# Kernel tuning notes

Measured on AMD Instinct MI355X. Metric: run time of the kernel, lower is better.

Reference implementation:

```python
import jax, jax.numpy as jnp
import numpy as np

B, S, N_EMBD = 4, 4096, 1024
HIDDEN = 4 * N_EMBD
M_BITS_FC = 3
M_BITS_PROJ = 3
BLOCK_K = 32


def block_quant(v, m_bits, bk):
    """Block-floating-point quantization along the last (K) dim.
    Each block of `bk` elements shares an exponent derived from its max-abs;
    mantissas are rounded to `m_bits` bits. Straight-through estimator for grads."""
    *lead, K = v.shape
    vb = v.reshape(*lead, K // bk, bk)
    amax = jnp.max(jnp.abs(vb), axis=-1, keepdims=True)
    tiny = jnp.asarray(2.0 ** -126, v.dtype)
    e = jnp.floor(jnp.log2(jnp.maximum(amax, tiny)))  # shared block exponent
    scale = jnp.exp2(e - m_bits)                       # quantization step
    q = jnp.round(vb / scale) * scale
    q = vb + jax.lax.stop_gradient(q - vb)             # STE
    return q.reshape(v.shape)


def lowprec_linear(x, w, b, m_bits, bk):
    # w: [out, in]; quantize both operands along the contraction dim.
    xq = block_quant(x, m_bits, bk)
    wq = block_quant(w, m_bits, bk)
    return jnp.einsum('bsk,nk->bsn', xq, wq) + b


def setup_inputs() -> dict:
    key = jax.random.key(0)
    k0, k1, k2 = jax.random.split(key, 3)
    x = jax.random.normal(k0, (B, S, N_EMBD), jnp.float32)
    w_fc = jax.random.normal(k1, (HIDDEN, N_EMBD), jnp.float32) * (1.0 / np.sqrt(N_EMBD))
    b_fc = jnp.zeros((HIDDEN,), jnp.float32)
    w_proj = jax.random.normal(k2, (N_EMBD, HIDDEN), jnp.float32) * (1.0 / np.sqrt(HIDDEN))
    b_proj = jnp.zeros((N_EMBD,), jnp.float32)
    return {"x": x, "w_fc": w_fc, "b_fc": b_fc, "w_proj": w_proj, "b_proj": b_proj}


def reference(x, w_fc, b_fc, w_proj, b_proj):
    h = lowprec_linear(x, w_fc, b_fc, M_BITS_FC, BLOCK_K)
    h = jax.nn.gelu(h, approximate=False)  # nn.GELU default = exact erf
    return lowprec_linear(h, w_proj, b_proj, M_BITS_PROJ, BLOCK_K)
```

## Files before the change

### kernel.cpp

```cpp
#include <hip/hip_runtime.h>
#include <hip/hip_bf16.h>

using bf16 = __hip_bfloat16;
typedef __attribute__((ext_vector_type(8))) short short8;
typedef __attribute__((ext_vector_type(4))) float f32x4;

#define DI __device__ __forceinline__

constexpr int MROWS = 16384;
constexpr int EMB   = 1024;
constexpr int HID   = 4096;

DI void gload16(const bf16* g, bf16* l) {
  __builtin_amdgcn_global_load_lds((const __attribute__((address_space(1))) void*)g,
                                   (__attribute__((address_space(3))) void*)l,
                                   16, 0, 0);
}

DI void qparams(float amax, float& scale, float& inv) {
  int eb = (int)((__float_as_uint(amax) >> 23) & 255u);
  eb = eb < 4 ? 4 : eb;
  scale = __uint_as_float((unsigned)(eb - 3) << 23);
  inv   = __uint_as_float((unsigned)(257 - eb) << 23);
}

__global__ void quant32(const float* __restrict__ in, bf16* __restrict__ out, int nblk) {
  int b = blockIdx.x * blockDim.x + threadIdx.x;
  if (b >= nblk) return;
  const float4* p = (const float4*)(in + (size_t)b * 32);
  float4 v[8];
  float amax = 0.f;
#pragma unroll
  for (int i = 0; i < 8; i++) {
    v[i] = p[i];
    amax = fmaxf(amax, fmaxf(fmaxf(fabsf(v[i].x), fabsf(v[i].y)),
                             fmaxf(fabsf(v[i].z), fabsf(v[i].w))));
  }
  float scale, inv;
  qparams(amax, scale, inv);
  alignas(16) unsigned short us[32];
#pragma unroll
  for (int i = 0; i < 8; i++) {
    us[i * 4 + 0] = (unsigned short)(__float_as_uint(rintf(v[i].x * inv) * scale) >> 16);
    us[i * 4 + 1] = (unsigned short)(__float_as_uint(rintf(v[i].y * inv) * scale) >> 16);
    us[i * 4 + 2] = (unsigned short)(__float_as_uint(rintf(v[i].z * inv) * scale) >> 16);
    us[i * 4 + 3] = (unsigned short)(__float_as_uint(rintf(v[i].w * inv) * scale) >> 16);
  }
  short8* o = (short8*)(out + (size_t)b * 32);
#pragma unroll
  for (int i = 0; i < 4; i++) o[i] = *(short8*)(us + i * 8);
}

#define MFMA16(a, b, c) __builtin_amdgcn_mfma_f32_16x16x32_bf16(a, b, c, 0, 0, 0)
#define SBAR()    __builtin_amdgcn_s_barrier()
#define WAITVM(n) asm volatile("s_waitcnt vmcnt(" #n ")" ::: "memory")

#define Q_MFMA(MB, NB, BG) \
  __builtin_amdgcn_s_setprio(1); \
  _Pragma("unroll") for (int kk = 0; kk < 2; kk++) \
  _Pragma("unroll") for (int mi = 0; mi < 4; mi++) \
  _Pragma("unroll") for (int ni = 0; ni < 2; ni++) \
    acc[(MB) + mi][(NB) + ni] = MFMA16(af[mi * 2 + kk], BG[ni * 2 + kk], acc[(MB) + mi][(NB) + ni]); \
  __builtin_amdgcn_s_setprio(0);

#define RD_AF(mh) \
  _Pragma("unroll") for (int mi = 0; mi < 4; mi++) { \
    af[mi * 2]     = ldA(db, mh, mi, 0); \
    af[mi * 2 + 1] = ldA(db, mh, mi, 1); }

#define RD_B(half, dst) \
  _Pragma("unroll") for (int ni = 0; ni < 2; ni++) { \
    dst[ni * 2]     = ldB(db, half, ni, 0); \
    dst[ni * 2 + 1] = ldB(db, half, ni, 1); }

template<int Kd, int Nd, bool GQ>
__global__ void __launch_bounds__(512, 2)
gemm8(const bf16* __restrict__ Ap, const bf16* __restrict__ Bp,
      const float* __restrict__ bias, void* __restrict__ Cout) {
  __shared__ alignas(16) bf16 SH[65536];
  bf16* Abuf = SH;
  bf16* Bbuf = SH + 32768;

  const int tid  = threadIdx.x;
  const int lane = tid & 63, wave = tid >> 6;
  const int l16  = lane & 15, lhi = lane >> 4;
  const int wr   = wave >> 2, wc  = wave & 3;

  const int idx  = blockIdx.x >> 3;
  const int xid  = blockIdx.x & 7;
  const int brow = (xid * 8 + (idx & 7)) * 256;
  const int bcol = (idx >> 3) * 256;

  const int r0 = tid >> 3;
  const int sl = (tid & 7) ^ (r0 & 7);
  const bf16* asrc = Ap + (size_t)(brow + r0) * Kd + sl * 8;
  const bf16* bsrc = Bp + (size_t)(bcol + r0) * Kd + sl * 8;

  auto stA = [&](int tt, int half) {
    const bf16* s = asrc + (size_t)half * 128 * Kd + tt * 64;
    bf16* d = Abuf + ((tt & 1) * 2 + half) * 8192 + tid * 8;
    gload16(s, d); gload16(s + (size_t)64 * Kd, d + 4096);
  };
  auto stB = [&](int tt, int half) {
    const bf16* s = bsrc + (size_t)half * 128 * Kd + tt * 64;
    bf16* d = Bbuf + ((tt & 1) * 2 + half) * 8192 + tid * 8;
    gload16(s, d); gload16(s + (size_t)64 * Kd, d + 4096);
  };

  const int sx = l16 & 7;
  const int arow = wr * 16 + l16;
  auto ldA = [&](int db, int mh, int mi, int kk) -> short8 {
    return *(const short8*)(Abuf + (db * 2 + mh) * 8192 +
                            (mi * 32 + arow) * 64 + ((kk * 4 + lhi) ^ sx) * 8);
  };
  const int brl = wc * 32 + l16;
  auto ldB = [&](int db, int half, int ni, int kk) -> short8 {
    return *(const short8*)(Bbuf + (db * 2 + half) * 8192 +
                            (brl + ni * 16) * 64 + ((kk * 4 + lhi) ^ sx) * 8);
  };

  f32x4 acc[8][4] = {};
  short8 af[8], bgl[4], bgh[4];

  constexpr int NT = Kd / 64;

  stA(0, 0); stB(0, 0); stB(0, 1); stA(0, 1);
  stA(1, 0); stB(1, 0); stB(1, 1);
  WAITVM(6); SBAR();

  for (int t = 0; t <= NT - 3; ++t) {
    const int db = t & 1;
    RD_AF(0) RD_B(0, bgl) RD_B(1, bgh)
    stA(t + 1, 1);
    Q_MFMA(0, 0, bgl)
    stA(t + 2, 0);
    Q_MFMA(0, 2, bgh)
    stB(t + 2, 0);
    RD_AF(1)
    stB(t + 2, 1);
    Q_MFMA(4, 0, bgl)
    Q_MFMA(4, 2, bgh)
    WAITVM(6); SBAR();
  }

  {
    const int db = (NT - 2) & 1;
    RD_AF(0) RD_B(0, bgl) RD_B(1, bgh)
    stA(NT - 1, 1);
    Q_MFMA(0, 0, bgl)
    Q_MFMA(0, 2, bgh)
    RD_AF(1)
    Q_MFMA(4, 0, bgl)
    Q_MFMA(4, 2, bgh)
    WAITVM(0); SBAR();
  }

  {
    const int db = (NT - 1) & 1;
    RD_AF(0) RD_B(0, bgl) RD_B(1, bgh)
    Q_MFMA(0, 0, bgl)
    Q_MFMA(0, 2, bgh)
    RD_AF(1)
    Q_MFMA(4, 0, bgl)
    Q_MFMA(4, 2, bgh)
  }

  const int cb = bcol + wc * 32;
  float bv[4];
#pragma unroll
  for (int n = 0; n < 4; n++) bv[n] = bias[cb + (n >> 1) * 128 + (n & 1) * 16 + l16];

  if constexpr (GQ) {
    SBAR();
#pragma unroll
    for (int m = 0; m < 8; m++) {
      const int rl0 = m * 32 + wr * 16 + lhi * 4;
#pragma unroll
      for (int r = 0; r < 4; r++) {
        float g[4];
#pragma unroll
        for (int n = 0; n < 4; n++) {
          float v = acc[m][n][r] + bv[n];
          g[n] = 0.5f * v * (1.0f + erff(v * 0.70710678118654752f));
        }
#pragma unroll
        for (int p = 0; p < 2; p++) {
          float am = fmaxf(fabsf(g[p * 2]), fabsf(g[p * 2 + 1]));
#pragma unroll
          for (int msk = 1; msk <= 8; msk <<= 1) am = fmaxf(am, __shfl_xor(am, msk, 64));
          float sc, iv; qparams(am, sc, iv);
          const int rowb = (rl0 + r) * 256;
          const int c0   = wc * 32 + p * 128;
          SH[rowb + ((c0 + l16)      ^ (lhi << 3))] = __float2bfloat16(rintf(g[p * 2]     * iv) * sc);
          SH[rowb + ((c0 + 16 + l16) ^ (lhi << 3))] = __float2bfloat16(rintf(g[p * 2 + 1] * iv) * sc);
        }
      }
    }
    SBAR();
    bf16* outp = (bf16*)Cout;
#pragma unroll
    for (int i = 0; i < 16; i++) {
      const int c   = i * 512 + tid;
      const int row = c >> 5, cc = c & 31;
      const int scc = cc ^ ((row >> 2) & 3);
      *(short8*)(outp + (size_t)(brow + row) * Nd + bcol + cc * 8) =
          *(const short8*)(SH + (size_t)row * 256 + scc * 8);
    }
  } else {
    float* outp = (float*)Cout;
#pragma unroll
    for (int m = 0; m < 8; m++) {
      const size_t rbase = (size_t)(brow + m * 32 + wr * 16 + lhi * 4);
#pragma unroll
      for (int r = 0; r < 4; r++) {
        const size_t ro = (rbase + r) * Nd;
#pragma unroll
        for (int n = 0; n < 4; n++)
          outp[ro + cb + (n >> 1) * 128 + (n & 1) * 16 + l16] = acc[m][n][r] + bv[n];
      }
    }
  }
}

extern "C" void kernel_launch(void* const* d_in, const int* in_sizes, int n_in,
                              void* d_out, int out_size, void* d_ws, size_t ws_size,
                              hipStream_t stream) {
  const float* x      = (const float*)d_in[0];
  const float* w_fc   = (const float*)d_in[1];
  const float* b_fc   = (const float*)d_in[2];
  const float* w_proj = (const float*)d_in[3];
  const float* b_proj = (const float*)d_in[4];

  char* ws = (char*)d_ws;
  bf16* xq  = (bf16*)ws;  ws += (size_t)MROWS * EMB * 2;
  bf16* wfq = (bf16*)ws;  ws += (size_t)HID * EMB * 2;
  bf16* wpq = (bf16*)ws;  ws += (size_t)EMB * HID * 2;
  bf16* hq  = (bf16*)ws;

  quant32<<<(MROWS * EMB / 32 + 255) / 256, 256, 0, stream>>>(x, xq, MROWS * EMB / 32);
  quant32<<<(HID * EMB / 32 + 255) / 256, 256, 0, stream>>>(w_fc, wfq, HID * EMB / 32);
  quant32<<<(EMB * HID / 32 + 255) / 256, 256, 0, stream>>>(w_proj, wpq, EMB * HID / 32);

  gemm8<EMB, HID, true ><<<(MROWS / 256) * (HID / 256), 512, 0, stream>>>(xq, wfq, b_fc, hq);
  gemm8<HID, EMB, false><<<(MROWS / 256) * (EMB / 256), 512, 0, stream>>>(hq, wpq, b_proj, (float*)d_out);
}
```

Measured before the change: 344.9 us.

## Use DPP reductions, split GELU epilogue staging, change swizzle, nontemporal output stores

The fused GELU+quant epilogue now does its 16-lane block max with DPP row operations instead of shuffles. It writes the bf16 tile to LDS in two 128-row halves with a wider XOR swizzle (lhi<<4), which should cut LDS bank conflicts. The final fp32 output of the second GEMM uses nontemporal stores to avoid polluting the cache, and the quant kernel is rewritten with vector-type indexing. Each change trims epilogue cost, but splitting the staging into halves adds an extra barrier pair.

New measurement: 335.4 us. 2.8% less time.

```diff
diff --git a/kernel.cpp b/kernel.cpp
--- a/kernel.cpp
+++ b/kernel.cpp
@@ -27,25 +27,23 @@
 __global__ void quant32(const float* __restrict__ in, bf16* __restrict__ out, int nblk) {
   int b = blockIdx.x * blockDim.x + threadIdx.x;
   if (b >= nblk) return;
-  const float4* p = (const float4*)(in + (size_t)b * 32);
-  float4 v[8];
+  const f32x4* p = (const f32x4*)(in + (size_t)b * 32);
+  f32x4 v[8];
   float amax = 0.f;
 #pragma unroll
   for (int i = 0; i < 8; i++) {
     v[i] = p[i];
-    amax = fmaxf(amax, fmaxf(fmaxf(fabsf(v[i].x), fabsf(v[i].y)),
-                             fmaxf(fabsf(v[i].z), fabsf(v[i].w))));
+    amax = fmaxf(amax, fmaxf(fmaxf(fabsf(v[i][0]), fabsf(v[i][1])),
+                             fmaxf(fabsf(v[i][2]), fabsf(v[i][3]))));
   }
   float scale, inv;
   qparams(amax, scale, inv);
   alignas(16) unsigned short us[32];
 #pragma unroll
-  for (int i = 0; i < 8; i++) {
-    us[i * 4 + 0] = (unsigned short)(__float_as_uint(rintf(v[i].x * inv) * scale) >> 16);
-    us[i * 4 + 1] = (unsigned short)(__float_as_uint(rintf(v[i].y * inv) * scale) >> 16);
-    us[i * 4 + 2] = (unsigned short)(__float_as_uint(rintf(v[i].z * inv) * scale) >> 16);
-    us[i * 4 + 3] = (unsigned short)(__float_as_uint(rintf(v[i].w * inv) * scale) >> 16);
-  }
+  for (int i = 0; i < 8; i++)
+#pragma unroll
+    for (int j = 0; j < 4; j++)
+      us[i * 4 + j] = (unsigned short)(__float_as_uint(rintf(v[i][j] * inv) * scale) >> 16);
   short8* o = (short8*)(out + (size_t)b * 32);
 #pragma unroll
   for (int i = 0; i < 4; i++) o[i] = *(short8*)(us + i * 8);
@@ -54,6 +52,14 @@
 #define MFMA16(a, b, c) __builtin_amdgcn_mfma_f32_16x16x32_bf16(a, b, c, 0, 0, 0)
 #define SBAR()    __builtin_amdgcn_s_barrier()
 #define WAITVM(n) asm volatile("s_waitcnt vmcnt(" #n ")" ::: "memory")
+
+#define DPPMAX(x, ctrl) \
+  x = fmaxf(x, __int_as_float(__builtin_amdgcn_update_dpp( \
+          0, __float_as_int(x), ctrl, 0xf, 0xf, false)));
+DI float redmax16(float x) {
+  DPPMAX(x, 0xB1) DPPMAX(x, 0x4E) DPPMAX(x, 0x124) DPPMAX(x, 0x128)
+  return x;
+}
 
 #define Q_MFMA(MB, NB, BG) \
   __builtin_amdgcn_s_setprio(1); \
@@ -171,40 +177,42 @@
   for (int n = 0; n < 4; n++) bv[n] = bias[cb + (n >> 1) * 128 + (n & 1) * 16 + l16];
 
   if constexpr (GQ) {
-    SBAR();
-#pragma unroll
-    for (int m = 0; m < 8; m++) {
-      const int rl0 = m * 32 + wr * 16 + lhi * 4;
-#pragma unroll
-      for (int r = 0; r < 4; r++) {
-        float g[4];
-#pragma unroll
-        for (int n = 0; n < 4; n++) {
-          float v = acc[m][n][r] + bv[n];
-          g[n] = 0.5f * v * (1.0f + erff(v * 0.70710678118654752f));
-        }
-#pragma unroll
-        for (int p = 0; p < 2; p++) {
-          float am = fmaxf(fabsf(g[p * 2]), fabsf(g[p * 2 + 1]));
-#pragma unroll
-          for (int msk = 1; msk <= 8; msk <<= 1) am = fmaxf(am, __shfl_xor(am, msk, 64));
-          float sc, iv; qparams(am, sc, iv);
+    bf16* outp = (bf16*)Cout;
+#pragma unroll
+    for (int mh2 = 0; mh2 < 2; mh2++) {
+      __syncthreads();
+#pragma unroll
+      for (int mm = 0; mm < 4; mm++) {
+        const int m = mh2 * 4 + mm;
+        const int rl0 = mm * 32 + wr * 16 + lhi * 4;
+#pragma unroll
+        for (int r = 0; r < 4; r++) {
+          float g[4];
+#pragma unroll
+          for (int n = 0; n < 4; n++) {
+            float v = acc[m][n][r] + bv[n];
+            g[n] = 0.5f * v * (1.0f + erff(v * 0.70710678118654752f));
+          }
           const int rowb = (rl0 + r) * 256;
-          const int c0   = wc * 32 + p * 128;
-          SH[rowb + ((c0 + l16)      ^ (lhi << 3))] = __float2bfloat16(rintf(g[p * 2]     * iv) * sc);
-          SH[rowb + ((c0 + 16 + l16) ^ (lhi << 3))] = __float2bfloat16(rintf(g[p * 2 + 1] * iv) * sc);
+#pragma unroll
+          for (int p = 0; p < 2; p++) {
+            float am = redmax16(fmaxf(fabsf(g[p * 2]), fabsf(g[p * 2 + 1])));
+            float sc, iv; qparams(am, sc, iv);
+            const int c0 = wc * 32 + p * 128;
+            SH[rowb + ((c0 + l16)      ^ (lhi << 4))] = __float2bfloat16(rintf(g[p * 2]     * iv) * sc);
+            SH[rowb + ((c0 + 16 + l16) ^ (lhi << 4))] = __float2bfloat16(rintf(g[p * 2 + 1] * iv) * sc);
+          }
         }
       }
-    }
-    SBAR();
-    bf16* outp = (bf16*)Cout;
-#pragma unroll
-    for (int i = 0; i < 16; i++) {
-      const int c   = i * 512 + tid;
-      const int row = c >> 5, cc = c & 31;
-      const int scc = cc ^ ((row >> 2) & 3);
-      *(short8*)(outp + (size_t)(brow + row) * Nd + bcol + cc * 8) =
-          *(const short8*)(SH + (size_t)row * 256 + scc * 8);
+      __syncthreads();
+#pragma unroll
+      for (int i = 0; i < 8; i++) {
+        const int c   = i * 512 + tid;
+        const int row = c >> 5, cc = c & 31;
+        const int scc = cc ^ (((row >> 2) & 3) << 1);
+        *(short8*)(outp + (size_t)(brow + mh2 * 128 + row) * Nd + bcol + cc * 8) =
+            *(const short8*)(SH + (size_t)row * 256 + scc * 8);
+      }
     }
   } else {
     float* outp = (float*)Cout;
@@ -216,7 +224,8 @@
         const size_t ro = (rbase + r) * Nd;
 #pragma unroll
         for (int n = 0; n < 4; n++)
-          outp[ro + cb + (n >> 1) * 128 + (n & 1) * 16 + l16] = acc[m][n][r] + bv[n];
+          __builtin_nontemporal_store(acc[m][n][r] + bv[n],
+              &outp[ro + cb + (n >> 1) * 128 + (n & 1) * 16 + l16]);
       }
     }
   }
```
